# Kernel tuning notes

Hardware: AMD Instinct MI355X
Metric: run time of the kernel (lower is better)

## Reference

```python
import jax, jax.numpy as jnp
import numpy as np


def setup_inputs() -> dict:
    key = jax.random.key(0)
    k1, k2, k3, k4, k5 = jax.random.split(key, 5)
    N, E, D = 100000, 600000, 128
    h = jax.random.normal(k1, (N, D), dtype=jnp.float32)
    src = jax.random.randint(k2, (E,), 0, N, dtype=jnp.int64)
    dst = jax.random.randint(k3, (E,), 0, N, dtype=jnp.int64)
    W_w = jax.random.normal(k4, (D, D), dtype=jnp.float32) * (1.0 / np.sqrt(D))
    W_b = jax.random.normal(k5, (D,), dtype=jnp.float32) * 0.01
    return {"h": h, "src": src, "dst": dst, "W_w": W_w, "W_b": W_b}


def reference(h, src, dst, W_w, W_b):
    # Project all node features once (N x D GEMM), then gather per edge.
    # score_e = sum_d (W h[src_e] + b)_d * h[dst_e]_d
    Wh = h @ W_w.T + W_b            # [N, D]
    scores = jnp.sum(Wh[src] * h[dst], axis=-1)  # [E]
    return scores
```

## Files before the change

kernel.cpp:

```cpp
#include <hip/hip_runtime.h>
#include <hip/hip_bf16.h>

#define D 128

typedef __attribute__((ext_vector_type(8))) short bf16x8;
typedef __attribute__((ext_vector_type(4))) float f32x4;

__device__ __forceinline__ unsigned int f2bf_bits(float f) {
    union { float f; unsigned int u; } c; c.f = f;
    return (c.u + 0x7fffu + ((c.u >> 16) & 1u)) >> 16;
}
__device__ __forceinline__ unsigned int pack2bf(float a, float b) {
    union { __hip_bfloat162 h; unsigned int u; } c;
    c.h = __float22bfloat162_rn(make_float2(a, b));
    return c.u;
}
__device__ __forceinline__ float bf_lo(unsigned int u) {
    union { unsigned int u; float f; } c; c.u = u << 16; return c.f;
}
__device__ __forceinline__ float bf_hi(unsigned int u) {
    union { unsigned int u; float f; } c; c.u = u & 0xffff0000u; return c.f;
}

__device__ __forceinline__ float dot8(uint4 a, uint4 b, float acc) {
    acc = fmaf(bf_lo(a.x), bf_lo(b.x), acc);
    acc = fmaf(bf_hi(a.x), bf_hi(b.x), acc);
    acc = fmaf(bf_lo(a.y), bf_lo(b.y), acc);
    acc = fmaf(bf_hi(a.y), bf_hi(b.y), acc);
    acc = fmaf(bf_lo(a.z), bf_lo(b.z), acc);
    acc = fmaf(bf_hi(a.z), bf_hi(b.z), acc);
    acc = fmaf(bf_lo(a.w), bf_lo(b.w), acc);
    acc = fmaf(bf_hi(a.w), bf_hi(b.w), acc);
    return acc;
}

__global__ __launch_bounds__(256) void wh_mfma_kernel(
    const float* __restrict__ h, const float* __restrict__ W,
    const float* __restrict__ bias, ushort* __restrict__ Wh_bf,
    ushort* __restrict__ h_bf, int N, int numTiles)
{
    __shared__ alignas(16) unsigned char lds_h[64 * 256];
    __shared__ alignas(16) unsigned char lds_w[128 * 256];

    const int t = threadIdx.x;

#pragma unroll
    for (int it = 0; it < 16; ++it) {
        const int idx = t + 256 * it;
        const int row = idx >> 5;
        const int seg = idx & 31;
        const float4 x = reinterpret_cast<const float4*>(W)[idx];
        const uint2 p = make_uint2(pack2bf(x.x, x.y), pack2bf(x.z, x.w));
        const int boff = (seg * 8) ^ ((row & 7) << 4);
        *reinterpret_cast<uint2*>(&lds_w[row * 256 + boff]) = p;
    }

    const int lane = t & 63;
    const int wv   = t >> 6;
    const int lr   = lane & 15;
    const int g    = lane >> 4;

    const int srow[8] = {  (t + 0*256) >> 5, (t + 1*256) >> 5, (t + 2*256) >> 5,
                           (t + 3*256) >> 5, (t + 4*256) >> 5, (t + 5*256) >> 5,
                           (t + 6*256) >> 5, (t + 7*256) >> 5 };
    const int sseg = t & 31;

    float4 R[8];
    {
        const int nodeBase = blockIdx.x * 64;
#pragma unroll
        for (int it = 0; it < 8; ++it) {
            const int node = nodeBase + srow[it];
            R[it] = (node < N)
                ? reinterpret_cast<const float4*>(h)[(size_t)node * 32 + sseg]
                : make_float4(0.f, 0.f, 0.f, 0.f);
        }
    }

    for (int tile = blockIdx.x; tile < numTiles; tile += gridDim.x) {
        const int nodeBase = tile * 64;

#pragma unroll
        for (int it = 0; it < 8; ++it) {
            const int row = srow[it];
            const int node = nodeBase + row;
            const float4 x = R[it];
            const uint2 p = make_uint2(pack2bf(x.x, x.y), pack2bf(x.z, x.w));
            const int boff = (sseg * 8) ^ ((row & 7) << 4);
            *reinterpret_cast<uint2*>(&lds_h[row * 256 + boff]) = p;
            if (node < N)
                *reinterpret_cast<uint2*>(h_bf + (size_t)node * D + sseg * 4) = p;
        }
        __syncthreads();

        bf16x8 hfrag[4];
        {
            const int row = wv * 16 + lr;
#pragma unroll
            for (int kt = 0; kt < 4; ++kt) {
                const int boff = (kt * 64 + g * 16) ^ ((row & 7) << 4);
                hfrag[kt] = *reinterpret_cast<const bf16x8*>(&lds_h[row * 256 + boff]);
            }
        }

        const int ntile = tile + gridDim.x;
        if (ntile < numTiles) {
            const int nb = ntile * 64;
#pragma unroll
            for (int it = 0; it < 8; ++it) {
                const int node = nb + srow[it];
                R[it] = (node < N)
                    ? reinterpret_cast<const float4*>(h)[(size_t)node * 32 + sseg]
                    : make_float4(0.f, 0.f, 0.f, 0.f);
            }
        }

        const int node   = nodeBase + wv * 16 + lr;
        const bool nodeOk = node < N;
#pragma unroll
        for (int ct = 0; ct < 8; ++ct) {
            const int wbase = ct * 16;
            const float4 b4 = *reinterpret_cast<const float4*>(bias + wbase + g * 4);
            f32x4 acc = {b4.x, b4.y, b4.z, b4.w};
#pragma unroll
            for (int kt = 0; kt < 4; ++kt) {
                const int wrow = wbase + lr;
                const int boff = (kt * 64 + g * 16) ^ ((wrow & 7) << 4);
                const bf16x8 wfrag =
                    *reinterpret_cast<const bf16x8*>(&lds_w[wrow * 256 + boff]);
                acc = __builtin_amdgcn_mfma_f32_16x16x32_bf16(wfrag, hfrag[kt], acc, 0, 0, 0);
            }
            if (nodeOk) {
                const uint2 p = make_uint2(pack2bf(acc[0], acc[1]),
                                           pack2bf(acc[2], acc[3]));
                *reinterpret_cast<uint2*>(Wh_bf + (size_t)node * D + wbase + g * 4) = p;
            }
        }
        __syncthreads();
    }
}

__global__ __launch_bounds__(256) void edge_score_kernel(
    const ushort* __restrict__ Wh_bf, const ushort* __restrict__ h_bf,
    const int* __restrict__ src, const int* __restrict__ dst,
    float* __restrict__ out, int base, int lim)
{
    const long long t = (long long)blockIdx.x * blockDim.x + threadIdx.x;
    const int grp = (int)(t >> 3);
    const int l   = (int)(t & 7);
    const int e0  = base + grp * 2;
    if (e0 >= lim) return;
    const int e1 = e0 + 1;
    const bool has1 = e1 < lim;

    const int s0 = src[e0], d0 = dst[e0];
    const int s1 = has1 ? src[e1] : s0;
    const int d1 = has1 ? dst[e1] : d0;

    const uint4* A0 = reinterpret_cast<const uint4*>(Wh_bf + (size_t)s0 * D);
    const uint4* B0 = reinterpret_cast<const uint4*>(h_bf  + (size_t)d0 * D);
    const uint4* A1 = reinterpret_cast<const uint4*>(Wh_bf + (size_t)s1 * D);
    const uint4* B1 = reinterpret_cast<const uint4*>(h_bf  + (size_t)d1 * D);

    const uint4 a0a = A0[2 * l];
    const uint4 a0b = A0[2 * l + 1];
    const uint4 b0a = B0[2 * l];
    const uint4 b0b = B0[2 * l + 1];
    const uint4 a1a = A1[2 * l];
    const uint4 a1b = A1[2 * l + 1];
    const uint4 b1a = B1[2 * l];
    const uint4 b1b = B1[2 * l + 1];

    float acc0 = dot8(a0a, b0a, 0.f);
    acc0 = dot8(a0b, b0b, acc0);
    float acc1 = dot8(a1a, b1a, 0.f);
    acc1 = dot8(a1b, b1b, acc1);

#pragma unroll
    for (int m = 4; m > 0; m >>= 1) {
        acc0 += __shfl_xor(acc0, m, 64);
        acc1 += __shfl_xor(acc1, m, 64);
    }

    if (l == 0) {
        if (has1)
            *reinterpret_cast<float2*>(out + e0) = make_float2(acc0, acc1);
        else
            out[e0] = acc0;
    }
}

extern "C" void kernel_launch(void* const* d_in, const int* in_sizes, int n_in,
                              void* d_out, int out_size, void* d_ws, size_t ws_size,
                              hipStream_t stream)
{
    const float* h   = (const float*)d_in[0];
    const int*   src = (const int*)  d_in[1];
    const int*   dst = (const int*)  d_in[2];
    const float* W   = (const float*)d_in[3];
    const float* b   = (const float*)d_in[4];
    float* out = (float*)d_out;

    const int N = in_sizes[0] / D;
    const int E = in_sizes[1];

    ushort* Wh_bf = (ushort*)d_ws;
    ushort* h_bf  = (ushort*)d_ws + (size_t)N * D;

    {
        const int numTiles = (N + 63) / 64;
        const int blocks = numTiles < 768 ? numTiles : 768;
        wh_mfma_kernel<<<blocks, 256, 0, stream>>>(h, W, b, Wh_bf, h_bf, N, numTiles);
    }
    {
        const int Ehalf = (E / 2) & ~1;
        const long long tot0 = ((long long)Ehalf + 1) / 2 * 8;
        const long long tot1 = ((long long)(E - Ehalf) + 1) / 2 * 8;
        const int blk0 = (int)((tot0 + 255) / 256);
        const int blk1 = (int)((tot1 + 255) / 256);
        edge_score_kernel<<<blk0, 256, 0, stream>>>(Wh_bf, h_bf, src, dst, out, 0, Ehalf);
        edge_score_kernel<<<blk1, 256, 0, stream>>>(Wh_bf, h_bf, src, dst, out, Ehalf, E);
    }
}
```

Baseline: 149.1 us.

## Load MFMA h fragments straight from global, drop LDS staging and barriers

The GEMM kernel no longer stages h tiles through LDS. Each lane reads its own h row fragment directly from global memory and converts it to bf16 in registers, which removes both per-tile __syncthreads and the LDS buffer. The persistent grid cap rises from 768 to 1024 blocks, and the two edge-kernel launches are merged into one. The tradeoff is that each h element is now read from global memory twice (once for the h_bf copy and once for the fragment), which adds some load traffic that should mostly hit cache.

```diff
diff --git a/kernel.cpp b/kernel.cpp
--- a/kernel.cpp
+++ b/kernel.cpp
@@ -39,7 +39,6 @@
     const float* __restrict__ bias, ushort* __restrict__ Wh_bf,
     ushort* __restrict__ h_bf, int N, int numTiles)
 {
-    __shared__ alignas(16) unsigned char lds_h[64 * 256];
     __shared__ alignas(16) unsigned char lds_w[128 * 256];
 
     const int t = threadIdx.x;
@@ -54,6 +53,7 @@
         const int boff = (seg * 8) ^ ((row & 7) << 4);
         *reinterpret_cast<uint2*>(&lds_w[row * 256 + boff]) = p;
     }
+    __syncthreads();
 
     const int lane = t & 63;
     const int wv   = t >> 6;
@@ -82,25 +82,29 @@
 
 #pragma unroll
         for (int it = 0; it < 8; ++it) {
-            const int row = srow[it];
-            const int node = nodeBase + row;
+            const int node = nodeBase + srow[it];
             const float4 x = R[it];
-            const uint2 p = make_uint2(pack2bf(x.x, x.y), pack2bf(x.z, x.w));
-            const int boff = (sseg * 8) ^ ((row & 7) << 4);
-            *reinterpret_cast<uint2*>(&lds_h[row * 256 + boff]) = p;
-            if (node < N)
+            if (node < N) {
+                const uint2 p = make_uint2(pack2bf(x.x, x.y), pack2bf(x.z, x.w));
                 *reinterpret_cast<uint2*>(h_bf + (size_t)node * D + sseg * 4) = p;
-        }
-        __syncthreads();
-
+            }
+        }
+
+        const int fnode = nodeBase + wv * 16 + lr;
+        const int cnode = fnode < N ? fnode : N - 1;
+        const float4* hrow = reinterpret_cast<const float4*>(h + (size_t)cnode * D);
         bf16x8 hfrag[4];
-        {
-            const int row = wv * 16 + lr;
-#pragma unroll
-            for (int kt = 0; kt < 4; ++kt) {
-                const int boff = (kt * 64 + g * 16) ^ ((row & 7) << 4);
-                hfrag[kt] = *reinterpret_cast<const bf16x8*>(&lds_h[row * 256 + boff]);
-            }
+#pragma unroll
+        for (int kt = 0; kt < 4; ++kt) {
+            const int f0 = (kt * 32 + g * 8) >> 2;
+            const float4 a = hrow[f0];
+            const float4 b = hrow[f0 + 1];
+            union { bf16x8 v; unsigned int u[4]; } fr;
+            fr.u[0] = pack2bf(a.x, a.y);
+            fr.u[1] = pack2bf(a.z, a.w);
+            fr.u[2] = pack2bf(b.x, b.y);
+            fr.u[3] = pack2bf(b.z, b.w);
+            hfrag[kt] = fr.v;
         }
 
         const int ntile = tile + gridDim.x;
@@ -115,8 +119,7 @@
             }
         }
 
-        const int node   = nodeBase + wv * 16 + lr;
-        const bool nodeOk = node < N;
+        const bool nodeOk = fnode < N;
 #pragma unroll
         for (int ct = 0; ct < 8; ++ct) {
             const int wbase = ct * 16;
@@ -133,25 +136,24 @@
             if (nodeOk) {
                 const uint2 p = make_uint2(pack2bf(acc[0], acc[1]),
                                            pack2bf(acc[2], acc[3]));
-                *reinterpret_cast<uint2*>(Wh_bf + (size_t)node * D + wbase + g * 4) = p;
-            }
-        }
-        __syncthreads();
+                *reinterpret_cast<uint2*>(Wh_bf + (size_t)fnode * D + wbase + g * 4) = p;
+            }
+        }
     }
 }
 
 __global__ __launch_bounds__(256) void edge_score_kernel(
     const ushort* __restrict__ Wh_bf, const ushort* __restrict__ h_bf,
     const int* __restrict__ src, const int* __restrict__ dst,
-    float* __restrict__ out, int base, int lim)
+    float* __restrict__ out, int E)
 {
     const long long t = (long long)blockIdx.x * blockDim.x + threadIdx.x;
     const int grp = (int)(t >> 3);
     const int l   = (int)(t & 7);
-    const int e0  = base + grp * 2;
-    if (e0 >= lim) return;
+    const int e0  = grp * 2;
+    if (e0 >= E) return;
     const int e1 = e0 + 1;
-    const bool has1 = e1 < lim;
+    const bool has1 = e1 < E;
 
     const int s0 = src[e0], d0 = dst[e0];
     const int s1 = has1 ? src[e1] : s0;
@@ -209,16 +211,12 @@
 
     {
         const int numTiles = (N + 63) / 64;
-        const int blocks = numTiles < 768 ? numTiles : 768;
+        const int blocks = numTiles < 1024 ? numTiles : 1024;
         wh_mfma_kernel<<<blocks, 256, 0, stream>>>(h, W, b, Wh_bf, h_bf, N, numTiles);
     }
     {
-        const int Ehalf = (E / 2) & ~1;
-        const long long tot0 = ((long long)Ehalf + 1) / 2 * 8;
-        const long long tot1 = ((long long)(E - Ehalf) + 1) / 2 * 8;
-        const int blk0 = (int)((tot0 + 255) / 256);
-        const int blk1 = (int)((tot1 + 255) / 256);
-        edge_score_kernel<<<blk0, 256, 0, stream>>>(Wh_bf, h_bf, src, dst, out, 0, Ehalf);
-        edge_score_kernel<<<blk1, 256, 0, stream>>>(Wh_bf, h_bf, src, dst, out, Ehalf, E);
-    }
-}
+        const long long total = ((long long)E + 1) / 2 * 8;
+        const int blocks = (int)((total + 255) / 256);
+        edge_score_kernel<<<blocks, 256, 0, stream>>>(Wh_bf, h_bf, src, dst, out, E);
+    }
+}
```

Result: no change. 148.7 us (-0.2%).
